# Kernel optimization log

Hardware: AMD Instinct MI355X
Metric: run time of the kernel (lower is better)

## Reference

```python
import jax, jax.numpy as jnp
import numpy as np

C_QKV = 128
C_HID = 32
N_HEADS = 4
INF = 1e9


def setup_inputs() -> dict:
    key = jax.random.key(0)
    ks = jax.random.split(key, 8)
    B, S = 256, 256
    hc = N_HEADS * C_HID  # 128
    inp = {
        "input_qkv": jax.random.normal(ks[0], (1, B, S, C_QKV), dtype=jnp.float32),
        "mask": jnp.ones((1, B, 1, 1, S), dtype=jnp.float32),
        "bias": jax.random.normal(ks[1], (1, 1, N_HEADS, S, S), dtype=jnp.float32),
        "add_transposed_output_to": jax.random.normal(ks[2], (1, B, S, C_QKV), dtype=jnp.float32),
        # linear_qkvg: Linear(c_qkv, 4*h*c), bias=False -> weight [4*hc, c_qkv]
        "W_qkvg": jax.random.normal(ks[3], (4 * hc, C_QKV), dtype=jnp.float32) * (1.0 / np.sqrt(C_QKV)),
        # gating bias initialized to ones in the module
        "linear_g_bias": jnp.ones((hc,), dtype=jnp.float32),
        # linear_o: Linear(hc, c_qkv), init='final' (zeros in AF2, use small random for a nontrivial test)
        "W_o": jax.random.normal(ks[4], (C_QKV, hc), dtype=jnp.float32) * (1.0 / np.sqrt(hc)),
        "b_o": jax.random.normal(ks[5], (C_QKV,), dtype=jnp.float32) * 0.02,
    }
    return inp


def reference(input_qkv, mask, bias, add_transposed_output_to, W_qkvg, linear_g_bias, W_o, b_o):
    hc = N_HEADS * C_HID
    # fused QKVG projection: [1, b, s, 4*hc]
    qkvg = jnp.einsum("xbsc,fc->xbsf", input_qkv, W_qkvg)
    q, k, v, g = jnp.split(qkvg, 4, axis=-1)
    # reshape to heads: [1, b, s, h, c]
    shp = q.shape[:-1] + (N_HEADS, C_HID)
    q = q.reshape(shp)
    k = k.reshape(shp)
    v = v.reshape(shp)
    scale = 1.0 / np.sqrt(C_HID)
    # scores: [1, b, h, q, k]
    a = jnp.einsum("xbqhc,xbkhc->xbhqk", q * scale, k)
    a = a + (mask - 1.0) * INF + bias
    a = jax.nn.softmax(a, axis=-1)
    # attention output: [1, b, q, h, c] -> [1, b, s, hc]
    o = jnp.einsum("xbhqk,xbkhc->xbqhc", a, v)
    o = o.reshape(o.shape[:-2] + (hc,))
    # sigmoid gating
    o = o * jax.nn.sigmoid(g + linear_g_bias)
    # fused linear + transpose(-2,-3) + add
    proj = jnp.einsum("xbsf,of->xbso", o, W_o) + b_o  # [1, b, s, c_qkv]
    out = add_transposed_output_to + jnp.swapaxes(proj, -2, -3)  # [1, s, b, c_qkv]
    return out
```

## Files before the change

kernel.cpp:

```cpp
#include <hip/hip_runtime.h>
#include <math.h>

#define BB 256
#define SS 256
#define NH 4

typedef __attribute__((ext_vector_type(8))) short bfrag;
typedef __attribute__((ext_vector_type(4))) float ffrag;

__device__ inline unsigned short f2bf(float x) {
    unsigned u = __float_as_uint(x);
    u += 0x7FFF + ((u >> 16) & 1);
    return (unsigned short)(u >> 16);
}
__device__ inline float bf2f(unsigned short h) {
    return __uint_as_float(((unsigned)h) << 16);
}
__device__ inline unsigned pack2(float a, float b) {
    return (unsigned)f2bf(a) | ((unsigned)f2bf(b) << 16);
}
__device__ inline unsigned cvt_pk_bf16(float lo, float hi) {
    unsigned r;
    asm("v_cvt_pk_bf16_f32 %0, %1, %2" : "=v"(r) : "v"(lo), "v"(hi));
    return r;
}
union FragU { unsigned u[4]; bfrag b; };

__device__ inline bfrag load_cvt_frag(const float* __restrict__ p) {
    const float4 a = *(const float4*)p;
    const float4 b = *(const float4*)(p + 4);
    FragU fu;
    fu.u[0] = cvt_pk_bf16(a.x, a.y);
    fu.u[1] = cvt_pk_bf16(a.z, a.w);
    fu.u[2] = cvt_pk_bf16(b.x, b.y);
    fu.u[3] = cvt_pk_bf16(b.z, b.w);
    return fu.b;
}

#define OG_OFF 0

__global__ __launch_bounds__(256, 2) void k_fused(
    const float* __restrict__ X,
    const float* __restrict__ W,
    const float* __restrict__ gbias,
    const float* __restrict__ mask,
    const float* __restrict__ bias,
    unsigned short* __restrict__ og)
{
    const int h = blockIdx.x, b = blockIdx.y;
    const int t = threadIdx.x;
    const int w = t >> 6, lane = t & 63, l15 = lane & 15, quad = lane >> 4;

    __shared__ unsigned short Qb[SS * 40];
    __shared__ unsigned short Kb[SS * 40];
    __shared__ unsigned short Vt[32 * 264];
    __shared__ unsigned short Gb[SS * 34];
    __shared__ float maskLds[SS];

    maskLds[t] = (mask[b * SS + t] - 1.0f) * 1e9f;

    const float qscale = 0.17677669529663687f;

    for (int half = 0; half < 2; ++half) {
        bfrag Wfr[4][4];
#pragma unroll
        for (int f4 = 0; f4 < 4; ++f4) {
            const int floc = (half * 4 + f4) * 16 + l15;
            const int grow = (floc >> 5) * 128 + h * 32 + (floc & 31);
#pragma unroll
            for (int cc = 0; cc < 4; ++cc)
                Wfr[f4][cc] = load_cvt_frag(W + grow * 128 + cc * 32 + quad * 8);
        }
#pragma unroll
        for (int st = 0; st < 4; ++st) {
            const int s = w * 64 + st * 16 + l15;
            bfrag Xfr[4];
#pragma unroll
            for (int cc = 0; cc < 4; ++cc)
                Xfr[cc] = load_cvt_frag(X + (b * SS + s) * 128 + cc * 32 + quad * 8);
#pragma unroll
            for (int f4 = 0; f4 < 4; ++f4) {
                ffrag D = {0.f, 0.f, 0.f, 0.f};
#pragma unroll
                for (int cc = 0; cc < 4; ++cc)
                    D = __builtin_amdgcn_mfma_f32_16x16x32_bf16(Xfr[cc], Wfr[f4][cc], D, 0, 0, 0);
                const int ft = half * 4 + f4;
                const int fcol = ft * 16 + l15;
                const int srow0 = w * 64 + st * 16 + quad * 4;
                if (ft < 2) {
#pragma unroll
                    for (int r = 0; r < 4; ++r)
                        Qb[(srow0 + r) * 40 + fcol] = f2bf(D[r] * qscale);
                } else if (ft < 4) {
#pragma unroll
                    for (int r = 0; r < 4; ++r)
                        Kb[(srow0 + r) * 40 + (fcol - 32)] = f2bf(D[r]);
                } else if (ft < 6) {
                    const int base = (fcol - 64) * 264 + srow0;
                    *(unsigned*)&Vt[base]     = pack2(D[0], D[1]);
                    *(unsigned*)&Vt[base + 2] = pack2(D[2], D[3]);
                } else {
                    const int c = fcol - 96;
                    const float gb = gbias[h * 32 + c];
#pragma unroll
                    for (int r = 0; r < 4; ++r) {
                        const float g = 1.0f / (1.0f + __expf(-(D[r] + gb)));
                        Gb[(srow0 + r) * 34 + c] = f2bf(g);
                    }
                }
            }
        }
    }
    __syncthreads();

    bfrag Vfr[2][8];
#pragma unroll
    for (int ch = 0; ch < 2; ++ch)
#pragma unroll
        for (int ck = 0; ck < 8; ++ck)
            Vfr[ch][ck] = *(const bfrag*)&Vt[(ch * 16 + l15) * 264 + ck * 32 + quad * 8];

    const int srcA = l15 + ((quad & 1) * 2) * 16;
    const int srcB = srcA + 16;
    const bool hi = (quad >> 1) != 0;

    for (int qq = 0; qq < 4; ++qq) {
        const int q = w * 64 + qq * 16 + l15;
        const bfrag Qfr = *(const bfrag*)&Qb[q * 40 + quad * 8];

        ffrag S[16];
#pragma unroll
        for (int kt = 0; kt < 16; ++kt) {
            const bfrag Kfr = *(const bfrag*)&Kb[(kt * 16 + l15) * 40 + quad * 8];
            const ffrag z = {0.f, 0.f, 0.f, 0.f};
            S[kt] = __builtin_amdgcn_mfma_f32_16x16x32_bf16(Kfr, Qfr, z, 0, 0, 0);
        }

        const float* brow = bias + (h * SS + q) * SS;
        float m = -1e30f;
#pragma unroll
        for (int kt = 0; kt < 16; ++kt) {
            const float4 bv = *(const float4*)(brow + kt * 16 + quad * 4);
            const float4 mv = *(const float4*)(maskLds + kt * 16 + quad * 4);
            S[kt][0] += bv.x + mv.x; S[kt][1] += bv.y + mv.y;
            S[kt][2] += bv.z + mv.z; S[kt][3] += bv.w + mv.w;
            m = fmaxf(m, fmaxf(fmaxf(S[kt][0], S[kt][1]), fmaxf(S[kt][2], S[kt][3])));
        }
        m = fmaxf(m, __shfl_xor(m, 16, 64));
        m = fmaxf(m, __shfl_xor(m, 32, 64));

        float l = 0.f;
        unsigned pk[16][2];
#pragma unroll
        for (int kt = 0; kt < 16; ++kt) {
            const float p0 = __expf(S[kt][0] - m);
            const float p1 = __expf(S[kt][1] - m);
            const float p2 = __expf(S[kt][2] - m);
            const float p3 = __expf(S[kt][3] - m);
            l += (p0 + p1) + (p2 + p3);
            pk[kt][0] = pack2(p0, p1);
            pk[kt][1] = pack2(p2, p3);
        }
        l += __shfl_xor(l, 16, 64);
        l += __shfl_xor(l, 32, 64);

        ffrag O[2];
        O[0] = (ffrag){0.f, 0.f, 0.f, 0.f};
        O[1] = (ffrag){0.f, 0.f, 0.f, 0.f};
#pragma unroll
        for (int ck = 0; ck < 8; ++ck) {
            const unsigned a0 = (unsigned)__shfl((int)pk[2 * ck][0],     srcA, 64);
            const unsigned b0 = (unsigned)__shfl((int)pk[2 * ck + 1][0], srcA, 64);
            const unsigned a1 = (unsigned)__shfl((int)pk[2 * ck][1],     srcA, 64);
            const unsigned b1 = (unsigned)__shfl((int)pk[2 * ck + 1][1], srcA, 64);
            const unsigned a2 = (unsigned)__shfl((int)pk[2 * ck][0],     srcB, 64);
            const unsigned b2 = (unsigned)__shfl((int)pk[2 * ck + 1][0], srcB, 64);
            const unsigned a3 = (unsigned)__shfl((int)pk[2 * ck][1],     srcB, 64);
            const unsigned b3 = (unsigned)__shfl((int)pk[2 * ck + 1][1], srcB, 64);
            FragU fu;
            fu.u[0] = hi ? b0 : a0;
            fu.u[1] = hi ? b1 : a1;
            fu.u[2] = hi ? b2 : a2;
            fu.u[3] = hi ? b3 : a3;
            O[0] = __builtin_amdgcn_mfma_f32_16x16x32_bf16(Vfr[0][ck], fu.b, O[0], 0, 0, 0);
            O[1] = __builtin_amdgcn_mfma_f32_16x16x32_bf16(Vfr[1][ck], fu.b, O[1], 0, 0, 0);
        }

        const float invl = 1.0f / l;
        const unsigned short* gr = &Gb[q * 34];
        unsigned* orow = (unsigned*)(og + (b * SS + q) * 128 + h * 32);
#pragma unroll
        for (int ch = 0; ch < 2; ++ch) {
            const int c0 = ch * 16 + quad * 4;
            const float v0 = O[ch][0] * invl * bf2f(gr[c0 + 0]);
            const float v1 = O[ch][1] * invl * bf2f(gr[c0 + 1]);
            const float v2 = O[ch][2] * invl * bf2f(gr[c0 + 2]);
            const float v3 = O[ch][3] * invl * bf2f(gr[c0 + 3]);
            orow[(c0 >> 1) + 0] = pack2(v0, v1);
            orow[(c0 >> 1) + 1] = pack2(v2, v3);
        }
    }
}

__global__ __launch_bounds__(256, 4) void k3_proj(
    const unsigned short* __restrict__ ogb,
    const float* __restrict__ Wo,
    const float* __restrict__ bo,
    const float* __restrict__ addt,
    float* __restrict__ out)
{
    const int j = blockIdx.x, ih = blockIdx.y;
    const int t = threadIdx.x;
    const int w = t >> 6, lane = t & 63, l15 = lane & 15, quad = lane >> 4;

    __shared__ unsigned short OgS[128 * 136];

    {
        const int ss = t >> 1, hf = t & 1;
        const unsigned short* src = ogb + (((size_t)j * SS + ih * 128 + ss) * 128) + hf * 64;
        unsigned short* dst = &OgS[ss * 136 + hf * 64];
#pragma unroll
        for (int u = 0; u < 8; ++u)
            *(uint4*)(dst + u * 8) = *(const uint4*)(src + u * 8);
    }

    bfrag Wfr[2][4];
#pragma unroll
    for (int ctl = 0; ctl < 2; ++ctl) {
        const int crow = (w * 2 + ctl) * 16 + l15;
#pragma unroll
        for (int cc = 0; cc < 4; ++cc)
            Wfr[ctl][cc] = load_cvt_frag(Wo + crow * 128 + cc * 32 + quad * 8);
    }
    const float bo0 = bo[(w * 2 + 0) * 16 + l15];
    const float bo1 = bo[(w * 2 + 1) * 16 + l15];

    __syncthreads();

#pragma unroll
    for (int jt = 0; jt < 8; ++jt) {
        bfrag Ab[4];
#pragma unroll
        for (int cc = 0; cc < 4; ++cc)
            Ab[cc] = *(const bfrag*)&OgS[(jt * 16 + l15) * 136 + cc * 32 + quad * 8];

        ffrag D0 = {0.f, 0.f, 0.f, 0.f};
        ffrag D1 = {0.f, 0.f, 0.f, 0.f};
#pragma unroll
        for (int cc = 0; cc < 4; ++cc) {
            D0 = __builtin_amdgcn_mfma_f32_16x16x32_bf16(Ab[cc], Wfr[0][cc], D0, 0, 0, 0);
            D1 = __builtin_amdgcn_mfma_f32_16x16x32_bf16(Ab[cc], Wfr[1][cc], D1, 0, 0, 0);
        }

        const int c0 = (w * 2 + 0) * 16 + l15;
        const int c1 = (w * 2 + 1) * 16 + l15;
#pragma unroll
        for (int r = 0; r < 4; ++r) {
            const int s = ih * 128 + jt * 16 + quad * 4 + r;
            const size_t row = ((size_t)s * BB + j) * 128;
            out[row + c0] = D0[r] + bo0 + addt[row + c0];
            out[row + c1] = D1[r] + bo1 + addt[row + c1];
        }
    }
}

extern "C" void kernel_launch(void* const* d_in, const int* in_sizes, int n_in,
                              void* d_out, int out_size, void* d_ws, size_t ws_size,
                              hipStream_t stream) {
    const float* X     = (const float*)d_in[0];
    const float* mask  = (const float*)d_in[1];
    const float* bias  = (const float*)d_in[2];
    const float* addt  = (const float*)d_in[3];
    const float* Wqkvg = (const float*)d_in[4];
    const float* gbias = (const float*)d_in[5];
    const float* Wo    = (const float*)d_in[6];
    const float* bo    = (const float*)d_in[7];
    float* out = (float*)d_out;

    unsigned short* og = (unsigned short*)d_ws + OG_OFF;

    k_fused<<<dim3(NH, BB), 256, 0, stream>>>(X, Wqkvg, gbias, mask, bias, og);
    k3_proj<<<dim3(BB, 2), 256, 0, stream>>>(og, Wo, bo, addt, out);
}
```

Before: 258.2 us.

## Fuse attention and output projection into one kernel per batch row

Merges the attention kernel and the output projection kernel into a single 512-thread block per batch row. The block loops over the four heads and keeps the gated attention output in LDS instead of writing it to global workspace, then applies the Wo projection directly. This removes the global round trip of the intermediate and one kernel launch. In exchange, grid parallelism drops from 1024 to 256 blocks at one block per CU, heads are serialized with extra barriers, and the X fragments are reloaded for each head. The packed bf16 conversion instruction is also replaced by software rounding.

After: 250.4 us. 1.03x faster.

```diff
diff --git a/kernel.cpp b/kernel.cpp
--- a/kernel.cpp
+++ b/kernel.cpp
@@ -19,247 +19,226 @@
 __device__ inline unsigned pack2(float a, float b) {
     return (unsigned)f2bf(a) | ((unsigned)f2bf(b) << 16);
 }
-__device__ inline unsigned cvt_pk_bf16(float lo, float hi) {
-    unsigned r;
-    asm("v_cvt_pk_bf16_f32 %0, %1, %2" : "=v"(r) : "v"(lo), "v"(hi));
-    return r;
-}
 union FragU { unsigned u[4]; bfrag b; };
 
-__device__ inline bfrag load_cvt_frag(const float* __restrict__ p) {
+__device__ inline bfrag cvt8(const float* __restrict__ p) {
     const float4 a = *(const float4*)p;
-    const float4 b = *(const float4*)(p + 4);
+    const float4 c = *(const float4*)(p + 4);
     FragU fu;
-    fu.u[0] = cvt_pk_bf16(a.x, a.y);
-    fu.u[1] = cvt_pk_bf16(a.z, a.w);
-    fu.u[2] = cvt_pk_bf16(b.x, b.y);
-    fu.u[3] = cvt_pk_bf16(b.z, b.w);
+    fu.u[0] = pack2(a.x, a.y);
+    fu.u[1] = pack2(a.z, a.w);
+    fu.u[2] = pack2(c.x, c.y);
+    fu.u[3] = pack2(c.z, c.w);
     return fu.b;
 }
 
-#define OG_OFF 0
-
-__global__ __launch_bounds__(256, 2) void k_fused(
+#define QB_O   0
+#define KB_O   10240
+#define VT_O   20480
+#define GB_O   28928
+#define OGL_O  37632
+#define MASK_BYTE_OFF 144896
+#define DYN_LDS_BYTES 145920
+
+__global__ __launch_bounds__(512, 1) void k_all(
     const float* __restrict__ X,
     const float* __restrict__ W,
     const float* __restrict__ gbias,
     const float* __restrict__ mask,
     const float* __restrict__ bias,
-    unsigned short* __restrict__ og)
-{
-    const int h = blockIdx.x, b = blockIdx.y;
-    const int t = threadIdx.x;
-    const int w = t >> 6, lane = t & 63, l15 = lane & 15, quad = lane >> 4;
-
-    __shared__ unsigned short Qb[SS * 40];
-    __shared__ unsigned short Kb[SS * 40];
-    __shared__ unsigned short Vt[32 * 264];
-    __shared__ unsigned short Gb[SS * 34];
-    __shared__ float maskLds[SS];
-
-    maskLds[t] = (mask[b * SS + t] - 1.0f) * 1e9f;
-
-    const float qscale = 0.17677669529663687f;
-
-    for (int half = 0; half < 2; ++half) {
-        bfrag Wfr[4][4];
-#pragma unroll
-        for (int f4 = 0; f4 < 4; ++f4) {
-            const int floc = (half * 4 + f4) * 16 + l15;
-            const int grow = (floc >> 5) * 128 + h * 32 + (floc & 31);
-#pragma unroll
-            for (int cc = 0; cc < 4; ++cc)
-                Wfr[f4][cc] = load_cvt_frag(W + grow * 128 + cc * 32 + quad * 8);
-        }
-#pragma unroll
-        for (int st = 0; st < 4; ++st) {
-            const int s = w * 64 + st * 16 + l15;
-            bfrag Xfr[4];
-#pragma unroll
-            for (int cc = 0; cc < 4; ++cc)
-                Xfr[cc] = load_cvt_frag(X + (b * SS + s) * 128 + cc * 32 + quad * 8);
-#pragma unroll
-            for (int f4 = 0; f4 < 4; ++f4) {
-                ffrag D = {0.f, 0.f, 0.f, 0.f};
-#pragma unroll
-                for (int cc = 0; cc < 4; ++cc)
-                    D = __builtin_amdgcn_mfma_f32_16x16x32_bf16(Xfr[cc], Wfr[f4][cc], D, 0, 0, 0);
-                const int ft = half * 4 + f4;
-                const int fcol = ft * 16 + l15;
-                const int srow0 = w * 64 + st * 16 + quad * 4;
-                if (ft < 2) {
-#pragma unroll
-                    for (int r = 0; r < 4; ++r)
-                        Qb[(srow0 + r) * 40 + fcol] = f2bf(D[r] * qscale);
-                } else if (ft < 4) {
-#pragma unroll
-                    for (int r = 0; r < 4; ++r)
-                        Kb[(srow0 + r) * 40 + (fcol - 32)] = f2bf(D[r]);
-                } else if (ft < 6) {
-                    const int base = (fcol - 64) * 264 + srow0;
-                    *(unsigned*)&Vt[base]     = pack2(D[0], D[1]);
-                    *(unsigned*)&Vt[base + 2] = pack2(D[2], D[3]);
-                } else {
-                    const int c = fcol - 96;
-                    const float gb = gbias[h * 32 + c];
-#pragma unroll
-                    for (int r = 0; r < 4; ++r) {
-                        const float g = 1.0f / (1.0f + __expf(-(D[r] + gb)));
-                        Gb[(srow0 + r) * 34 + c] = f2bf(g);
-                    }
-                }
-            }
-        }
-    }
-    __syncthreads();
-
-    bfrag Vfr[2][8];
-#pragma unroll
-    for (int ch = 0; ch < 2; ++ch)
-#pragma unroll
-        for (int ck = 0; ck < 8; ++ck)
-            Vfr[ch][ck] = *(const bfrag*)&Vt[(ch * 16 + l15) * 264 + ck * 32 + quad * 8];
-
-    const int srcA = l15 + ((quad & 1) * 2) * 16;
-    const int srcB = srcA + 16;
-    const bool hi = (quad >> 1) != 0;
-
-    for (int qq = 0; qq < 4; ++qq) {
-        const int q = w * 64 + qq * 16 + l15;
-        const bfrag Qfr = *(const bfrag*)&Qb[q * 40 + quad * 8];
-
-        ffrag S[16];
-#pragma unroll
-        for (int kt = 0; kt < 16; ++kt) {
-            const bfrag Kfr = *(const bfrag*)&Kb[(kt * 16 + l15) * 40 + quad * 8];
-            const ffrag z = {0.f, 0.f, 0.f, 0.f};
-            S[kt] = __builtin_amdgcn_mfma_f32_16x16x32_bf16(Kfr, Qfr, z, 0, 0, 0);
-        }
-
-        const float* brow = bias + (h * SS + q) * SS;
-        float m = -1e30f;
-#pragma unroll
-        for (int kt = 0; kt < 16; ++kt) {
-            const float4 bv = *(const float4*)(brow + kt * 16 + quad * 4);
-            const float4 mv = *(const float4*)(maskLds + kt * 16 + quad * 4);
-            S[kt][0] += bv.x + mv.x; S[kt][1] += bv.y + mv.y;
-            S[kt][2] += bv.z + mv.z; S[kt][3] += bv.w + mv.w;
-            m = fmaxf(m, fmaxf(fmaxf(S[kt][0], S[kt][1]), fmaxf(S[kt][2], S[kt][3])));
-        }
-        m = fmaxf(m, __shfl_xor(m, 16, 64));
-        m = fmaxf(m, __shfl_xor(m, 32, 64));
-
-        float l = 0.f;
-        unsigned pk[16][2];
-#pragma unroll
-        for (int kt = 0; kt < 16; ++kt) {
-            const float p0 = __expf(S[kt][0] - m);
-            const float p1 = __expf(S[kt][1] - m);
-            const float p2 = __expf(S[kt][2] - m);
-            const float p3 = __expf(S[kt][3] - m);
-            l += (p0 + p1) + (p2 + p3);
-            pk[kt][0] = pack2(p0, p1);
-            pk[kt][1] = pack2(p2, p3);
-        }
-        l += __shfl_xor(l, 16, 64);
-        l += __shfl_xor(l, 32, 64);
-
-        ffrag O[2];
-        O[0] = (ffrag){0.f, 0.f, 0.f, 0.f};
-        O[1] = (ffrag){0.f, 0.f, 0.f, 0.f};
-#pragma unroll
-        for (int ck = 0; ck < 8; ++ck) {
-            const unsigned a0 = (unsigned)__shfl((int)pk[2 * ck][0],     srcA, 64);
-            const unsigned b0 = (unsigned)__shfl((int)pk[2 * ck + 1][0], srcA, 64);
-            const unsigned a1 = (unsigned)__shfl((int)pk[2 * ck][1],     srcA, 64);
-            const unsigned b1 = (unsigned)__shfl((int)pk[2 * ck + 1][1], srcA, 64);
-            const unsigned a2 = (unsigned)__shfl((int)pk[2 * ck][0],     srcB, 64);
-            const unsigned b2 = (unsigned)__shfl((int)pk[2 * ck + 1][0], srcB, 64);
-            const unsigned a3 = (unsigned)__shfl((int)pk[2 * ck][1],     srcB, 64);
-            const unsigned b3 = (unsigned)__shfl((int)pk[2 * ck + 1][1], srcB, 64);
-            FragU fu;
-            fu.u[0] = hi ? b0 : a0;
-            fu.u[1] = hi ? b1 : a1;
-            fu.u[2] = hi ? b2 : a2;
-            fu.u[3] = hi ? b3 : a3;
-            O[0] = __builtin_amdgcn_mfma_f32_16x16x32_bf16(Vfr[0][ck], fu.b, O[0], 0, 0, 0);
-            O[1] = __builtin_amdgcn_mfma_f32_16x16x32_bf16(Vfr[1][ck], fu.b, O[1], 0, 0, 0);
-        }
-
-        const float invl = 1.0f / l;
-        const unsigned short* gr = &Gb[q * 34];
-        unsigned* orow = (unsigned*)(og + (b * SS + q) * 128 + h * 32);
-#pragma unroll
-        for (int ch = 0; ch < 2; ++ch) {
-            const int c0 = ch * 16 + quad * 4;
-            const float v0 = O[ch][0] * invl * bf2f(gr[c0 + 0]);
-            const float v1 = O[ch][1] * invl * bf2f(gr[c0 + 1]);
-            const float v2 = O[ch][2] * invl * bf2f(gr[c0 + 2]);
-            const float v3 = O[ch][3] * invl * bf2f(gr[c0 + 3]);
-            orow[(c0 >> 1) + 0] = pack2(v0, v1);
-            orow[(c0 >> 1) + 1] = pack2(v2, v3);
-        }
-    }
-}
-
-__global__ __launch_bounds__(256, 4) void k3_proj(
-    const unsigned short* __restrict__ ogb,
     const float* __restrict__ Wo,
     const float* __restrict__ bo,
     const float* __restrict__ addt,
     float* __restrict__ out)
 {
-    const int j = blockIdx.x, ih = blockIdx.y;
+    const int b = blockIdx.x;
     const int t = threadIdx.x;
     const int w = t >> 6, lane = t & 63, l15 = lane & 15, quad = lane >> 4;
 
-    __shared__ unsigned short OgS[128 * 136];
-
-    {
-        const int ss = t >> 1, hf = t & 1;
-        const unsigned short* src = ogb + (((size_t)j * SS + ih * 128 + ss) * 128) + hf * 64;
-        unsigned short* dst = &OgS[ss * 136 + hf * 64];
-#pragma unroll
-        for (int u = 0; u < 8; ++u)
-            *(uint4*)(dst + u * 8) = *(const uint4*)(src + u * 8);
+    extern __shared__ unsigned short smem[];
+    unsigned short* Qb  = smem + QB_O;
+    unsigned short* Kb  = smem + KB_O;
+    unsigned short* Vt  = smem + VT_O;
+    unsigned short* Gb  = smem + GB_O;
+    unsigned short* ogL = smem + OGL_O;
+    float* maskLds = (float*)((char*)smem + MASK_BYTE_OFF);
+
+    if (t < SS) maskLds[t] = (mask[b * SS + t] - 1.0f) * 1e9f;
+
+    const float qscale = 0.17677669529663687f;
+
+    const int srcA = l15 + ((quad & 1) * 2) * 16;
+    const int srcB = srcA + 16;
+    const bool hi = (quad >> 1) != 0;
+
+    for (int h = 0; h < NH; ++h) {
+        __syncthreads();
+
+        bfrag Xf[2][4];
+#pragma unroll
+        for (int st = 0; st < 2; ++st) {
+            const int s = w * 32 + st * 16 + l15;
+#pragma unroll
+            for (int cc = 0; cc < 4; ++cc)
+                Xf[st][cc] = cvt8(X + (size_t)(b * SS + s) * 128 + cc * 32 + quad * 8);
+        }
+        for (int half = 0; half < 2; ++half) {
+            bfrag Wfr[4][4];
+#pragma unroll
+            for (int f4 = 0; f4 < 4; ++f4) {
+                const int floc = (half * 4 + f4) * 16 + l15;
+                const int grow = (floc >> 5) * 128 + h * 32 + (floc & 31);
+#pragma unroll
+                for (int cc = 0; cc < 4; ++cc)
+                    Wfr[f4][cc] = cvt8(W + (size_t)grow * 128 + cc * 32 + quad * 8);
+            }
+#pragma unroll
+            for (int st = 0; st < 2; ++st) {
+#pragma unroll
+                for (int f4 = 0; f4 < 4; ++f4) {
+                    ffrag D = {0.f, 0.f, 0.f, 0.f};
+#pragma unroll
+                    for (int cc = 0; cc < 4; ++cc)
+                        D = __builtin_amdgcn_mfma_f32_16x16x32_bf16(Xf[st][cc], Wfr[f4][cc], D, 0, 0, 0);
+                    const int ft = half * 4 + f4;
+                    const int fcol = ft * 16 + l15;
+                    const int srow0 = w * 32 + st * 16 + quad * 4;
+                    if (ft < 2) {
+#pragma unroll
+                        for (int r = 0; r < 4; ++r)
+                            Qb[(srow0 + r) * 40 + fcol] = f2bf(D[r] * qscale);
+                    } else if (ft < 4) {
+#pragma unroll
+                        for (int r = 0; r < 4; ++r)
+                            Kb[(srow0 + r) * 40 + (fcol - 32)] = f2bf(D[r]);
+                    } else if (ft < 6) {
+                        const int base = (fcol - 64) * 264 + srow0;
+                        *(unsigned*)&Vt[base]     = pack2(D[0], D[1]);
+                        *(unsigned*)&Vt[base + 2] = pack2(D[2], D[3]);
+                    } else {
+                        const int c = fcol - 96;
+                        const float gb = gbias[h * 32 + c];
+#pragma unroll
+                        for (int r = 0; r < 4; ++r) {
+                            const float g = 1.0f / (1.0f + __expf(-(D[r] + gb)));
+                            Gb[(srow0 + r) * 34 + c] = f2bf(g);
+                        }
+                    }
+                }
+            }
+        }
+        __syncthreads();
+
+        bfrag Vfr[2][8];
+#pragma unroll
+        for (int ch = 0; ch < 2; ++ch)
+#pragma unroll
+            for (int ck = 0; ck < 8; ++ck)
+                Vfr[ch][ck] = *(const bfrag*)&Vt[(ch * 16 + l15) * 264 + ck * 32 + quad * 8];
+
+        for (int qq = 0; qq < 2; ++qq) {
+            const int q = w * 32 + qq * 16 + l15;
+            const bfrag Qfr = *(const bfrag*)&Qb[q * 40 + quad * 8];
+
+            ffrag S[16];
+#pragma unroll
+            for (int kt = 0; kt < 16; ++kt) {
+                const bfrag Kfr = *(const bfrag*)&Kb[(kt * 16 + l15) * 40 + quad * 8];
+                const ffrag z = {0.f, 0.f, 0.f, 0.f};
+                S[kt] = __builtin_amdgcn_mfma_f32_16x16x32_bf16(Kfr, Qfr, z, 0, 0, 0);
+            }
+
+            const float* brow = bias + ((size_t)h * SS + q) * SS;
+            float m = -1e30f;
+#pragma unroll
+            for (int kt = 0; kt < 16; ++kt) {
+                const float4 bv = *(const float4*)(brow + kt * 16 + quad * 4);
+                const float4 mv = *(const float4*)(maskLds + kt * 16 + quad * 4);
+                S[kt][0] += bv.x + mv.x; S[kt][1] += bv.y + mv.y;
+                S[kt][2] += bv.z + mv.z; S[kt][3] += bv.w + mv.w;
+                m = fmaxf(m, fmaxf(fmaxf(S[kt][0], S[kt][1]), fmaxf(S[kt][2], S[kt][3])));
+            }
+            m = fmaxf(m, __shfl_xor(m, 16, 64));
+            m = fmaxf(m, __shfl_xor(m, 32, 64));
+
+            float l = 0.f;
+            unsigned pk[16][2];
+#pragma unroll
+            for (int kt = 0; kt < 16; ++kt) {
+                const float p0 = __expf(S[kt][0] - m);
+                const float p1 = __expf(S[kt][1] - m);
+                const float p2 = __expf(S[kt][2] - m);
+                const float p3 = __expf(S[kt][3] - m);
+                l += (p0 + p1) + (p2 + p3);
+                pk[kt][0] = pack2(p0, p1);
+                pk[kt][1] = pack2(p2, p3);
+            }
+            l += __shfl_xor(l, 16, 64);
+            l += __shfl_xor(l, 32, 64);
+
+            ffrag O[2];
+            O[0] = (ffrag){0.f, 0.f, 0.f, 0.f};
+            O[1] = (ffrag){0.f, 0.f, 0.f, 0.f};
+#pragma unroll
+            for (int ck = 0; ck < 8; ++ck) {
+                const unsigned a0 = (unsigned)__shfl((int)pk[2 * ck][0],     srcA, 64);
+                const unsigned b0 = (unsigned)__shfl((int)pk[2 * ck + 1][0], srcA, 64);
+                const unsigned a1 = (unsigned)__shfl((int)pk[2 * ck][1],     srcA, 64);
+                const unsigned b1 = (unsigned)__shfl((int)pk[2 * ck + 1][1], srcA, 64);
+                const unsigned a2 = (unsigned)__shfl((int)pk[2 * ck][0],     srcB, 64);
+                const unsigned b2 = (unsigned)__shfl((int)pk[2 * ck + 1][0], srcB, 64);
+                const unsigned a3 = (unsigned)__shfl((int)pk[2 * ck][1],     srcB, 64);
+                const unsigned b3 = (unsigned)__shfl((int)pk[2 * ck + 1][1], srcB, 64);
+                FragU fu;
+                fu.u[0] = hi ? b0 : a0;
+                fu.u[1] = hi ? b1 : a1;
+                fu.u[2] = hi ? b2 : a2;
+                fu.u[3] = hi ? b3 : a3;
+                O[0] = __builtin_amdgcn_mfma_f32_16x16x32_bf16(Vfr[0][ck], fu.b, O[0], 0, 0, 0);
+                O[1] = __builtin_amdgcn_mfma_f32_16x16x32_bf16(Vfr[1][ck], fu.b, O[1], 0, 0, 0);
+            }
+
+            const float invl = 1.0f / l;
+            const unsigned short* gr = &Gb[q * 34];
+            unsigned* orow = (unsigned*)&ogL[q * 136 + h * 32];
+#pragma unroll
+            for (int ch = 0; ch < 2; ++ch) {
+                const int c0 = ch * 16 + quad * 4;
+                const float v0 = O[ch][0] * invl * bf2f(gr[c0 + 0]);
+                const float v1 = O[ch][1] * invl * bf2f(gr[c0 + 1]);
+                const float v2 = O[ch][2] * invl * bf2f(gr[c0 + 2]);
+                const float v3 = O[ch][3] * invl * bf2f(gr[c0 + 3]);
+                orow[(c0 >> 1) + 0] = pack2(v0, v1);
+                orow[(c0 >> 1) + 1] = pack2(v2, v3);
+            }
+        }
     }
-
-    bfrag Wfr[2][4];
-#pragma unroll
-    for (int ctl = 0; ctl < 2; ++ctl) {
-        const int crow = (w * 2 + ctl) * 16 + l15;
+    __syncthreads();
+
+    const int crow = w * 16 + l15;
+    bfrag Wofr[4];
+#pragma unroll
+    for (int cc = 0; cc < 4; ++cc)
+        Wofr[cc] = cvt8(Wo + (size_t)crow * 128 + cc * 32 + quad * 8);
+    const float boc = bo[crow];
+
+#pragma unroll
+    for (int jt = 0; jt < 16; ++jt) {
+        bfrag Ab[4];
 #pragma unroll
         for (int cc = 0; cc < 4; ++cc)
-            Wfr[ctl][cc] = load_cvt_frag(Wo + crow * 128 + cc * 32 + quad * 8);
-    }
-    const float bo0 = bo[(w * 2 + 0) * 16 + l15];
-    const float bo1 = bo[(w * 2 + 1) * 16 + l15];
-
-    __syncthreads();
-
-#pragma unroll
-    for (int jt = 0; jt < 8; ++jt) {
-        bfrag Ab[4];
+            Ab[cc] = *(const bfrag*)&ogL[(jt * 16 + l15) * 136 + cc * 32 + quad * 8];
+
+        ffrag D = {0.f, 0.f, 0.f, 0.f};
 #pragma unroll
         for (int cc = 0; cc < 4; ++cc)
-            Ab[cc] = *(const bfrag*)&OgS[(jt * 16 + l15) * 136 + cc * 32 + quad * 8];
-
-        ffrag D0 = {0.f, 0.f, 0.f, 0.f};
-        ffrag D1 = {0.f, 0.f, 0.f, 0.f};
-#pragma unroll
-        for (int cc = 0; cc < 4; ++cc) {
-            D0 = __builtin_amdgcn_mfma_f32_16x16x32_bf16(Ab[cc], Wfr[0][cc], D0, 0, 0, 0);
-            D1 = __builtin_amdgcn_mfma_f32_16x16x32_bf16(Ab[cc], Wfr[1][cc], D1, 0, 0, 0);
-        }
-
-        const int c0 = (w * 2 + 0) * 16 + l15;
-        const int c1 = (w * 2 + 1) * 16 + l15;
+            D = __builtin_amdgcn_mfma_f32_16x16x32_bf16(Ab[cc], Wofr[cc], D, 0, 0, 0);
+
 #pragma unroll
         for (int r = 0; r < 4; ++r) {
-            const int s = ih * 128 + jt * 16 + quad * 4 + r;
-            const size_t row = ((size_t)s * BB + j) * 128;
-            out[row + c0] = D0[r] + bo0 + addt[row + c0];
-            out[row + c1] = D1[r] + bo1 + addt[row + c1];
+            const int s = jt * 16 + quad * 4 + r;
+            const size_t off = ((size_t)s * BB + b) * 128 + crow;
+            out[off] = D[r] + boc + addt[off];
         }
     }
 }
@@ -277,8 +256,14 @@
     const float* bo    = (const float*)d_in[7];
     float* out = (float*)d_out;
 
-    unsigned short* og = (unsigned short*)d_ws + OG_OFF;
-
-    k_fused<<<dim3(NH, BB), 256, 0, stream>>>(X, Wqkvg, gbias, mask, bias, og);
-    k3_proj<<<dim3(BB, 2), 256, 0, stream>>>(og, Wo, bo, addt, out);
-}
+    static bool attrDone = false;
+    if (!attrDone) {
+        hipFuncSetAttribute((const void*)k_all,
+                            hipFuncAttributeMaxDynamicSharedMemorySize,
+                            DYN_LDS_BYTES);
+        attrDone = true;
+    }
+
+    k_all<<<BB, 512, DYN_LDS_BYTES, stream>>>(X, Wqkvg, gbias, mask, bias,
+                                              Wo, bo, addt, out);
+}
```
